# Optimization experiments

Measured on AMD Instinct MI355X. Metric: run time of the kernel, lower is better.

## Reference

```python
import jax, jax.numpy as jnp
import numpy as np

B, FEW, NN = 4096, 5, 64
D = 128            # embed_dim
NSYM = 100000
DM = 2 * D         # d_model = 256
DI = 2 * DM        # support-encoder inner = 512
H = 2 * DM         # LSTMCell hidden = 512
STEPS = 4          # process_steps


def setup_inputs() -> dict:
    key = jax.random.key(0)
    cnt = [0]
    def nk():
        cnt[0] += 1
        return jax.random.fold_in(key, cnt[0])
    def nrm(shape, scale=0.05):
        return jax.random.normal(nk(), shape, dtype=jnp.float32) * scale
    def ridx(shape):
        return jax.random.randint(nk(), shape, 0, NSYM, dtype=jnp.int32)
    inp = {}
    inp['q_l1'] = ridx((B, NN, 2)); inp['q_l2'] = ridx((B, NN, 2))
    inp['q_r1'] = ridx((B, NN, 2)); inp['q_r2'] = ridx((B, NN, 2))
    inp['s_l1'] = ridx((FEW, NN, 2)); inp['s_l2'] = ridx((FEW, NN, 2))
    inp['s_r1'] = ridx((FEW, NN, 2)); inp['s_r2'] = ridx((FEW, NN, 2))
    inp['q_deg_l'] = jax.random.randint(nk(), (B,), 1, NN, dtype=jnp.int32)
    inp['q_deg_r'] = jax.random.randint(nk(), (B,), 1, NN, dtype=jnp.int32)
    inp['s_deg_l'] = jax.random.randint(nk(), (FEW,), 1, NN, dtype=jnp.int32)
    inp['s_deg_r'] = jax.random.randint(nk(), (FEW,), 1, NN, dtype=jnp.int32)
    inp['emb'] = nrm((NSYM + 1, D)).at[NSYM].set(0.0)  # padding_idx row = 0
    inp['gcn_w'] = nrm((D, 2 * D))
    inp['gcn_wb'] = nrm((D,))
    inp['gcn_b'] = jnp.zeros((D,), jnp.float32)
    inp['hop_gate'] = jnp.ones((2,), jnp.float32)
    inp['attn_w'] = nrm((1, D))
    inp['attn_b'] = jnp.zeros((1,), jnp.float32)
    inp['p1_w'] = nrm((DI, DM)); inp['p1_b'] = jnp.zeros((DI,), jnp.float32)
    inp['p2_w'] = nrm((DM, DI)); inp['p2_b'] = jnp.zeros((DM,), jnp.float32)
    inp['ln_g'] = jnp.ones((DM,), jnp.float32); inp['ln_b'] = jnp.zeros((DM,), jnp.float32)
    inp['w_ih'] = nrm((4 * H, DM)); inp['w_hh'] = nrm((4 * H, H))
    inp['b_ih'] = jnp.zeros((4 * H,), jnp.float32); inp['b_hh'] = jnp.zeros((4 * H,), jnp.float32)
    return inp


def _neighbor_encoder(conn, emb, gcn_w, gcn_wb, gcn_b, attn_w, attn_b):
    # conn: [N, NN, 2] (relation id, entity id)
    e = emb[conn]                                     # [N, NN, 2, D]
    concat = e.reshape(conn.shape[0], conn.shape[1], 2 * D)  # cat(rel, ent)
    proj = concat @ gcn_w.T + gcn_wb + gcn_b          # [N, NN, D]
    scores = (proj @ attn_w.T + attn_b)[..., 0]       # [N, NN]
    w = jax.nn.softmax(scores, axis=1)[..., None]
    return jnp.tanh(jnp.sum(proj * w, axis=1))        # [N, D]


def _support_encoder(x, p1_w, p1_b, p2_w, p2_b, ln_g, ln_b):
    out = jax.nn.relu(x @ p1_w.T + p1_b) @ p2_w.T + p2_b
    z = out + x
    mu = jnp.mean(z, axis=-1, keepdims=True)
    var = jnp.var(z, axis=-1, keepdims=True)
    return (z - mu) / jnp.sqrt(var + 1e-6) * ln_g + ln_b


def _query_encoder(support_g, q, w_ih, w_hh, b_ih, b_hh):
    # matching-networks 'process' LSTM attention, STEPS fixed iterations
    h_r = jnp.zeros((q.shape[0], H), q.dtype)
    c = jnp.zeros_like(h_r)
    h = q
    for _ in range(STEPS):
        gates = q @ w_ih.T + b_ih + h_r @ w_hh.T + b_hh
        i, f, g, o = jnp.split(gates, 4, axis=-1)
        c = jax.nn.sigmoid(f) * c + jax.nn.sigmoid(i) * jnp.tanh(g)
        h_cell = jax.nn.sigmoid(o) * jnp.tanh(c)
        h = q + h_cell[:, :DM]
        attn = jax.nn.softmax(h @ support_g.T, axis=1)
        r = attn @ support_g
        h_r = jnp.concatenate([h, r], axis=1)
    return h


def reference(q_l1, q_l2, q_r1, q_r2, s_l1, s_l2, s_r1, s_r2,
              q_deg_l, q_deg_r, s_deg_l, s_deg_r,
              emb, gcn_w, gcn_wb, gcn_b, hop_gate, attn_w, attn_b,
              p1_w, p1_b, p2_w, p2_b, ln_g, ln_b, w_ih, w_hh, b_ih, b_hh):
    ne = lambda conn: _neighbor_encoder(conn, emb, gcn_w, gcn_wb, gcn_b, attn_w, attn_b)
    gw = jax.nn.softmax(hop_gate)
    q_left = gw[0] * ne(q_l1) + gw[1] * ne(q_l2)
    q_right = gw[0] * ne(q_r1) + gw[1] * ne(q_r2)
    s_left = gw[0] * ne(s_l1) + gw[1] * ne(s_l2)
    s_right = gw[0] * ne(s_r1) + gw[1] * ne(s_r2)
    query_neighbor = jnp.concatenate([q_left, q_right], axis=-1)    # [B, DM]
    support_neighbor = jnp.concatenate([s_left, s_right], axis=-1)  # [FEW, DM]
    support_g = _support_encoder(support_neighbor, p1_w, p1_b, p2_w, p2_b, ln_g, ln_b)
    query_g = _query_encoder(support_g, query_neighbor, w_ih, w_hh, b_ih, b_hh)
    support_m = jnp.mean(support_g, axis=0, keepdims=True)          # [1, DM]
    return (query_g @ support_m.T)[:, 0]                            # [B]
```

## Files before the change

kernel.cpp:

```cpp
#include <hip/hip_runtime.h>

typedef unsigned short bf16u;
typedef unsigned char u8;
typedef unsigned int u32;
typedef float f32x4 __attribute__((ext_vector_type(4)));
typedef short bf16x8 __attribute__((ext_vector_type(8)));

__device__ inline float sigmoidf_(float x) { return 1.f / (1.f + __expf(-x)); }
__device__ inline float tanhf_(float x) {
  float e = __expf(2.f * x);
  return 1.f - 2.f / (e + 1.f);
}
__device__ inline float b2f(bf16u u) { return __uint_as_float(((u32)u) << 16); }
__device__ inline bf16u f2b(float f) {
  u32 i = __float_as_uint(f);
  u32 r = (i + 0x7fffu + ((i >> 16) & 1u)) >> 16;
  return (bf16u)r;
}
__device__ inline u8 enc8(float v) {
  float q = fmaf(v, 512.f, 128.5f);
  q = fminf(fmaxf(q, 0.f), 255.f);
  return (u8)(int)q;
}
__device__ inline float ub0(u32 u) { return (float)(u & 0xffu); }
__device__ inline float ub1(u32 u) { return (float)((u >> 8) & 0xffu); }
__device__ inline float ub2(u32 u) { return (float)((u >> 16) & 0xffu); }
__device__ inline float ub3(u32 u) { return (float)(u >> 24); }

#define GLOAD16(gsrc, ldst)                                                   \
  __builtin_amdgcn_global_load_lds(                                           \
      (const __attribute__((address_space(1))) void*)(gsrc),                  \
      (__attribute__((address_space(3))) void*)(ldst), 16, 0, 0)

__global__ __launch_bounds__(256) void k_prep(
    const float* __restrict__ gcn_w, const float* __restrict__ attn_w,
    const float* __restrict__ w_ih, const float* __restrict__ w_hh,
    const float* __restrict__ b_ih, const float* __restrict__ b_hh,
    bf16u* __restrict__ Vp, float* __restrict__ uvec,
    bf16u* __restrict__ WWa, bf16u* __restrict__ WWb, float* __restrict__ bsum,
    bf16u* __restrict__ XX)
{
  const int b = blockIdx.x, t = threadIdx.x;
  if (t < 59) XX[(size_t)b * 576 + 517 + t] = 0;
  if (b < 2048) {
    float wi = w_ih[b * 256 + t];
    float wh = w_hh[b * 512 + t];
    WWa[(size_t)b * 576 + t] = f2b(wi);
    WWb[(size_t)b * 576 + t] = f2b(wi + wh);
    WWb[(size_t)b * 576 + 256 + t] = f2b(wh);
    if (t < 59) WWb[(size_t)b * 576 + 517 + t] = 0;
    if (t == 0) bsum[b] = b_ih[b] + b_hh[b];
  } else if (b < 2304) {
    const int o = b - 2048;
    if (t < 128) Vp[o * 128 + t] = f2b(gcn_w[(o & 127) * 256 + ((o >> 7) << 7) + t]);
  } else if (b == 2304) {
    const int col = ((t >> 7) << 7) + (t & 127);
    float acc = 0.f;
    for (int d = 0; d < 128; ++d) acc += gcn_w[d * 256 + col] * attn_w[d];
    uvec[t] = acc;
  }
}

__global__ __launch_bounds__(256) void k_pre_gemm(
    const float* __restrict__ emb, const bf16u* __restrict__ Vp,
    const float* __restrict__ uvec,
    u8* __restrict__ pr, u8* __restrict__ pe,
    float* __restrict__ srel, float* __restrict__ sent)
{
  const int t = threadIdx.x;
  const int row0 = blockIdx.x << 6;
  __shared__ short As[64][136];
  __shared__ union PB {
    short B[128][136];
    u8 ob[64][272];
  } pb;
  __shared__ float us[256];
  us[t] = uvec[t];
  {
    const uint4* src = (const uint4*)Vp;
    #pragma unroll
    for (int s = 0; s < 8; ++s) {
      int f = s * 256 + t;
      *(uint4*)&pb.B[f >> 4][(f & 15) * 8] = src[f];
    }
  }
  #pragma unroll
  for (int s = 0; s < 8; ++s) {
    int f = s * 256 + t;
    int row = f >> 5, q = f & 31;
    int gr = row0 + row; if (gr > 100000) gr = 100000;
    float4 v = *(const float4*)&emb[(size_t)gr * 128 + (q << 2)];
    ushort4 pk;
    pk.x = f2b(v.x); pk.y = f2b(v.y); pk.z = f2b(v.z); pk.w = f2b(v.w);
    *(ushort4*)&As[row][q << 2] = pk;
  }
  __syncthreads();
  {
    const int row = t >> 2, l = t & 3;
    int gr = row0 + row; if (gr > 100000) gr = 100000;
    const short* ar = &As[row][l * 32];
    const float* u0 = &us[l * 32];
    const float* u1 = &us[128 + l * 32];
    float p0 = 0.f, p1 = 0.f;
    #pragma unroll
    for (int i = 0; i < 32; ++i) {
      float e = __uint_as_float(((u32)(unsigned short)ar[i]) << 16);
      p0 += e * u0[i];
      p1 += e * u1[i];
    }
    p0 += __shfl_xor(p0, 1, 64); p0 += __shfl_xor(p0, 2, 64);
    p1 += __shfl_xor(p1, 1, 64); p1 += __shfl_xor(p1, 2, 64);
    if (l == 0) { srel[gr] = p0; sent[gr] = p1; }
  }
  const int wave = t >> 6, lane = t & 63;
  const int quad = lane >> 4, l16 = lane & 15;
  const int wm = (wave >> 1) << 5, wn = (wave & 1) << 6;
  f32x4 acc0[2][4], acc1[2][4];
  #pragma unroll
  for (int i = 0; i < 2; ++i)
    #pragma unroll
    for (int j = 0; j < 4; ++j) {
      acc0[i][j] = (f32x4){0.f, 0.f, 0.f, 0.f};
      acc1[i][j] = (f32x4){0.f, 0.f, 0.f, 0.f};
    }
  #pragma unroll
  for (int kc = 0; kc < 4; ++kc) {
    bf16x8 af[2], bfr[4];
    #pragma unroll
    for (int i = 0; i < 2; ++i)
      af[i] = *(const bf16x8*)&As[wm + i * 16 + l16][kc * 32 + quad * 8];
    #pragma unroll
    for (int j = 0; j < 4; ++j)
      bfr[j] = *(const bf16x8*)&pb.B[wn + j * 16 + l16][kc * 32 + quad * 8];
    #pragma unroll
    for (int i = 0; i < 2; ++i)
      #pragma unroll
      for (int j = 0; j < 4; ++j)
        acc0[i][j] = __builtin_amdgcn_mfma_f32_16x16x32_bf16(af[i], bfr[j], acc0[i][j], 0, 0, 0);
  }
  __syncthreads();
  {
    const uint4* src = (const uint4*)(Vp + 128 * 128);
    #pragma unroll
    for (int s = 0; s < 8; ++s) {
      int f = s * 256 + t;
      *(uint4*)&pb.B[f >> 4][(f & 15) * 8] = src[f];
    }
  }
  __syncthreads();
  #pragma unroll
  for (int kc = 0; kc < 4; ++kc) {
    bf16x8 af[2], bfr[4];
    #pragma unroll
    for (int i = 0; i < 2; ++i)
      af[i] = *(const bf16x8*)&As[wm + i * 16 + l16][kc * 32 + quad * 8];
    #pragma unroll
    for (int j = 0; j < 4; ++j)
      bfr[j] = *(const bf16x8*)&pb.B[wn + j * 16 + l16][kc * 32 + quad * 8];
    #pragma unroll
    for (int i = 0; i < 2; ++i)
      #pragma unroll
      for (int j = 0; j < 4; ++j)
        acc1[i][j] = __builtin_amdgcn_mfma_f32_16x16x32_bf16(af[i], bfr[j], acc1[i][j], 0, 0, 0);
  }
  __syncthreads();
  #pragma unroll
  for (int j = 0; j < 4; ++j) {
    const int col = wn + j * 16 + l16;
    #pragma unroll
    for (int i = 0; i < 2; ++i) {
      #pragma unroll
      for (int r = 0; r < 4; ++r) {
        int row = wm + i * 16 + quad * 4 + r;
        pb.ob[row][col] = enc8(acc0[i][j][r]);
        pb.ob[row][128 + col] = enc8(acc1[i][j][r]);
      }
    }
  }
  __syncthreads();
  #pragma unroll
  for (int s = 0; s < 4; ++s) {
    int c = s * 256 + t;
    int row = c >> 4, part = c & 15;
    int gr = row0 + row;
    if (gr <= 100000) {
      uint4 v = *(const uint4*)&pb.ob[row][part * 16];
      if (part < 8) *(uint4*)&pr[(size_t)gr * 128 + part * 16] = v;
      else          *(uint4*)&pe[(size_t)gr * 128 + (part - 8) * 16] = v;
    }
  }
}

__global__ __launch_bounds__(256) void k_neighbor(
    const int* __restrict__ q_l1, const int* __restrict__ q_l2,
    const int* __restrict__ q_r1, const int* __restrict__ q_r2,
    const int* __restrict__ s_l1, const int* __restrict__ s_l2,
    const int* __restrict__ s_r1, const int* __restrict__ s_r2,
    const u8* __restrict__ pr, const u8* __restrict__ pe,
    const float* __restrict__ srel, const float* __restrict__ sent,
    const float* __restrict__ gcn_wb, const float* __restrict__ gcn_b,
    const float* __restrict__ hop_gate,
    float* __restrict__ qn, float* __restrict__ sn, bf16u* __restrict__ XX)
{
  const int b = blockIdx.x, t = threadIdx.x;
  const int *cA, *cB; float* outp; bf16u* xxp; int n, coloff;
  if (b < 4096)      { cA = q_l1; cB = q_l2; n = b;        outp = qn; xxp = XX; coloff = 0; }
  else if (b < 8192) { cA = q_r1; cB = q_r2; n = b - 4096; outp = qn; xxp = XX; coloff = 128; }
  else if (b < 8197) { cA = s_l1; cB = s_l2; n = b - 8192; outp = sn; xxp = 0;  coloff = 0; }
  else               { cA = s_r1; cB = s_r2; n = b - 8197; outp = sn; xxp = 0;  coloff = 128; }

  __shared__ float wS[2][64];
  __shared__ float red[256][17];

  const int hop = t >> 7, g = (t >> 3) & 15, p = t & 7;
  const int* connG = hop ? cB : cA;

  int2 pairs[4];
  #pragma unroll
  for (int kk = 0; kk < 4; ++kk)
    pairs[kk] = *(const int2*)&connG[(n * 64 + g + (kk << 4)) * 2];

  float vR = 0.f, vE = 0.f;
  if (t < 128) {
    const int sh = t >> 6, nn = t & 63;
    const int* connS = sh ? cB : cA;
    int2 sp = *(const int2*)&connS[(n * 64 + nn) * 2];
    vR = srel[sp.x];
    vE = sent[sp.y];
  }

  uint4 ra[4], rb[4];
  #pragma unroll
  for (int kk = 0; kk < 4; ++kk) {
    ra[kk] = *(const uint4*)&pr[(size_t)pairs[kk].x * 128 + p * 16];
    rb[kk] = *(const uint4*)&pe[(size_t)pairs[kk].y * 128 + p * 16];
  }

  if (t < 128) {
    const int sh = t >> 6, nn = t & 63;
    float sc = vR + vE;
    float m = sc;
    #pragma unroll
    for (int off = 32; off; off >>= 1) m = fmaxf(m, __shfl_xor(m, off, 64));
    float e = __expf(sc - m);
    float s = e;
    #pragma unroll
    for (int off = 32; off; off >>= 1) s += __shfl_xor(s, off, 64);
    wS[sh][nn] = e / s;
  }
  __syncthreads();

  float a[16];
  #pragma unroll
  for (int c = 0; c < 16; ++c) a[c] = 0.f;
  #pragma unroll
  for (int kk = 0; kk < 4; ++kk) {
    const float wk = wS[hop][g + (kk << 4)];
    const uint4 A = ra[kk], Bv = rb[kk];
    a[0]  += wk * (ub0(A.x) + ub0(Bv.x));
    a[1]  += wk * (ub1(A.x) + ub1(Bv.x));
    a[2]  += wk * (ub2(A.x) + ub2(Bv.x));
    a[3]  += wk * (ub3(A.x) + ub3(Bv.x));
    a[4]  += wk * (ub0(A.y) + ub0(Bv.y));
    a[5]  += wk * (ub1(A.y) + ub1(Bv.y));
    a[6]  += wk * (ub2(A.y) + ub2(Bv.y));
    a[7]  += wk * (ub3(A.y) + ub3(Bv.y));
    a[8]  += wk * (ub0(A.z) + ub0(Bv.z));
    a[9]  += wk * (ub1(A.z) + ub1(Bv.z));
    a[10] += wk * (ub2(A.z) + ub2(Bv.z));
    a[11] += wk * (ub3(A.z) + ub3(Bv.z));
    a[12] += wk * (ub0(A.w) + ub0(Bv.w));
    a[13] += wk * (ub1(A.w) + ub1(Bv.w));
    a[14] += wk * (ub2(A.w) + ub2(Bv.w));
    a[15] += wk * (ub3(A.w) + ub3(Bv.w));
  }
  #pragma unroll
  for (int c = 0; c < 16; ++c) red[t][c] = a[c];
  __syncthreads();

  if (t < 128) {
    const int d = t, pp = d >> 4, cc = d & 15;
    float sA = 0.f, sB = 0.f;
    #pragma unroll
    for (int gg = 0; gg < 16; ++gg) {
      sA += red[gg * 8 + pp][cc];
      sB += red[128 + gg * 8 + pp][cc];
    }
    float accA = sA * (1.f / 512.f) - 0.5f;
    float accB = sB * (1.f / 512.f) - 0.5f;
    float bias = gcn_wb[d] + gcn_b[d];
    float g0 = hop_gate[0], g1 = hop_gate[1];
    float mx = fmaxf(g0, g1);
    float e0 = __expf(g0 - mx), e1 = __expf(g1 - mx);
    float inv = 1.f / (e0 + e1);
    float v = e0 * inv * tanhf_(bias + accA) + e1 * inv * tanhf_(bias + accB);
    outp[n * 256 + coloff + d] = v;
    if (xxp) xxp[(size_t)n * 576 + coloff + d] = f2b(v);
  }
}

__global__ __launch_bounds__(256) void k_sup1(
    const float* __restrict__ sn, const float* __restrict__ p1_w,
    const float* __restrict__ p1_b, float* __restrict__ h1)
{
  const int r = blockIdx.x >> 3, j0 = (blockIdx.x & 7) << 6;
  const int t = threadIdx.x;
  __shared__ float xs[256];
  xs[t] = sn[r * 256 + t];
  __syncthreads();
  const int j = j0 + (t >> 2), q = t & 3;
  const float* wr = p1_w + (size_t)j * 256 + q * 64;
  float acc = 0.f;
  #pragma unroll
  for (int k = 0; k < 64; ++k) acc += xs[q * 64 + k] * wr[k];
  acc += __shfl_xor(acc, 1, 64);
  acc += __shfl_xor(acc, 2, 64);
  if (q == 0) h1[r * 512 + j] = fmaxf(acc + p1_b[j], 0.f);
}

__global__ __launch_bounds__(256) void k_sup2(
    const float* __restrict__ sn, const float* __restrict__ h1,
    const float* __restrict__ p2_w, const float* __restrict__ p2_b,
    const float* __restrict__ ln_g, const float* __restrict__ ln_b,
    float* __restrict__ sg)
{
  const int r = blockIdx.x, t = threadIdx.x;
  const int lane = t & 63, wave = t >> 6;
  __shared__ float hs[512];
  __shared__ float zs[256];
  __shared__ float r1[4], r2[4];
  hs[t] = h1[r * 512 + t];
  hs[t + 256] = h1[r * 512 + 256 + t];
  __syncthreads();
  const int q = t & 3;
  #pragma unroll
  for (int jc = 0; jc < 4; ++jc) {
    int j = jc * 64 + (t >> 2);
    const float* wr = p2_w + (size_t)j * 512 + q * 128;
    float acc = 0.f;
    #pragma unroll
    for (int k = 0; k < 128; ++k) acc += hs[q * 128 + k] * wr[k];
    acc += __shfl_xor(acc, 1, 64);
    acc += __shfl_xor(acc, 2, 64);
    if (q == 0) zs[j] = acc + p2_b[j] + sn[r * 256 + j];
  }
  __syncthreads();
  float v = zs[t];
  float s1 = v, s2 = v * v;
  #pragma unroll
  for (int off = 32; off; off >>= 1) { s1 += __shfl_xor(s1, off, 64); s2 += __shfl_xor(s2, off, 64); }
  if (lane == 0) { r1[wave] = s1; r2[wave] = s2; }
  __syncthreads();
  float S1 = r1[0] + r1[1] + r1[2] + r1[3];
  float S2 = r2[0] + r2[1] + r2[2] + r2[3];
  float mu = S1 * (1.f / 256.f);
  float var = S2 * (1.f / 256.f) - mu * mu;
  sg[r * 256 + t] = (v - mu) * rsqrtf(var + 1e-6f) * ln_g[t] + ln_b[t];
}

__global__ __launch_bounds__(256) void k_sg2(
    const float* __restrict__ sg, const float* __restrict__ w_hh,
    bf16u* __restrict__ WWb, float* __restrict__ sm)
{
  __shared__ float s[5][256];
  const int t = threadIdx.x;
  for (int i = t; i < 1280; i += 256) s[i >> 8][i & 255] = sg[i];
  __syncthreads();
  if (blockIdx.x == 0)
    sm[t] = (s[0][t] + s[1][t] + s[2][t] + s[3][t] + s[4][t]) * 0.2f;
  const int j = (blockIdx.x << 6) + (t >> 2), q = t & 3;
  const float4* wr = (const float4*)(w_hh + (size_t)j * 512 + 256 + q * 64);
  float a[5] = {0.f, 0.f, 0.f, 0.f, 0.f};
  #pragma unroll
  for (int kk = 0; kk < 16; ++kk) {
    float4 w = wr[kk];
    int k = q * 64 + kk * 4;
    #pragma unroll
    for (int r = 0; r < 5; ++r)
      a[r] += s[r][k] * w.x + s[r][k+1] * w.y + s[r][k+2] * w.z + s[r][k+3] * w.w;
  }
  #pragma unroll
  for (int r = 0; r < 5; ++r) {
    a[r] += __shfl_xor(a[r], 1, 64);
    a[r] += __shfl_xor(a[r], 2, 64);
  }
  if (q == 0) {
    #pragma unroll
    for (int r = 0; r < 5; ++r)
      WWb[(size_t)j * 576 + 512 + r] = f2b(a[r]);
  }
}

__global__ __launch_bounds__(256) void k_gates_mfma(
    const bf16u* __restrict__ XX, const bf16u* __restrict__ WW,
    const float* __restrict__ bsum, bf16u* __restrict__ gates, int kchunks)
{
  const int t = threadIdx.x;
  const int wave = t >> 6, lane = t & 63;
  const int quad = lane >> 4, l16 = lane & 15;
  const int wm = (wave >> 1) << 6, wn = (wave & 1) << 6;
  const int lin = (blockIdx.x & 7) * 56 + (blockIdx.x >> 3);
  const int row0 = (lin / 14) << 7;
  const int col0 = (lin % 14) << 7;
  __shared__ short As[2][128][32];
  __shared__ short Bs[2][128][32];
  f32x4 acc[4][4];
  #pragma unroll
  for (int i = 0; i < 4; ++i)
    #pragma unroll
    for (int j = 0; j < 4; ++j) acc[i][j] = (f32x4){0.f, 0.f, 0.f, 0.f};

  int offX[2], offW[2];
  #pragma unroll
  for (int e = 0; e < 2; ++e) {
    int s = wave * 128 + e * 64 + lane;
    int row = s >> 2, qs = s & 3;
    int sw = qs ^ ((row >> 1) & 3);
    offX[e] = (row0 + row) * 576 + sw * 8;
    offW[e] = (col0 + row) * 576 + sw * 8;
  }
  char* aBase = (char*)&As[0][0][0] + wave * 2048;
  char* bBase = (char*)&Bs[0][0][0] + wave * 2048;

  #define STAGE(buf, kc)                                                      \
    {                                                                         \
      const int kof_ = (kc) * 32;                                             \
      _Pragma("unroll")                                                       \
      for (int e = 0; e < 2; ++e) {                                           \
        GLOAD16(XX + offX[e] + kof_, aBase + (buf) * 8192 + e * 1024);        \
        GLOAD16(WW + offW[e] + kof_, bBase + (buf) * 8192 + e * 1024);        \
      }                                                                       \
    }

  STAGE(0, 0);
  __syncthreads();

  const int swq = (quad ^ ((l16 >> 1) & 3)) << 3;
  for (int kc = 0; kc < kchunks; ++kc) {
    const int cur = kc & 1;
    if (kc + 1 < kchunks) STAGE(cur ^ 1, kc + 1);
    bf16x8 af[4], bfr[4];
    #pragma unroll
    for (int i = 0; i < 4; ++i)
      af[i] = *(const bf16x8*)&As[cur][wm + i * 16 + l16][swq];
    #pragma unroll
    for (int j = 0; j < 4; ++j)
      bfr[j] = *(const bf16x8*)&Bs[cur][wn + j * 16 + l16][swq];
    #pragma unroll
    for (int i = 0; i < 4; ++i)
      #pragma unroll
      for (int j = 0; j < 4; ++j)
        acc[i][j] = __builtin_amdgcn_mfma_f32_16x16x32_bf16(af[i], bfr[j], acc[i][j], 0, 0, 0);
    __syncthreads();
  }
  #undef STAGE

  #pragma unroll
  for (int j = 0; j < 4; ++j) {
    const int col = col0 + wn + j * 16 + l16;
    const float bs = bsum[col];
    #pragma unroll
    for (int i = 0; i < 4; ++i) {
      #pragma unroll
      for (int r = 0; r < 4; ++r) {
        int row = row0 + wm + i * 16 + quad * 4 + r;
        gates[(size_t)row * 2048 + col] = f2b(acc[i][j][r] + bs);
      }
    }
  }
}

__global__ __launch_bounds__(256) void k_cell(
    const bf16u* __restrict__ gates, const float* __restrict__ qn,
    float* __restrict__ c, bf16u* __restrict__ XX,
    const float* __restrict__ sg, const float* __restrict__ sm,
    float* __restrict__ out, int step)
{
  __shared__ float red[4][6];
  const int b = blockIdx.x, t = threadIdx.x;
  const int lane = t & 63, wave = t >> 6;
  const bf16u* g = gates + (size_t)b * 2048;
  float i0 = b2f(g[t]),       f0 = b2f(g[512 + t]), gg0 = b2f(g[1024 + t]), o0 = b2f(g[1536 + t]);
  float i1 = b2f(g[256 + t]), f1 = b2f(g[768 + t]), gg1 = b2f(g[1280 + t]);
  float co0 = step ? c[b * 512 + t] : 0.f;
  float co1 = step ? c[b * 512 + 256 + t] : 0.f;
  float c0 = sigmoidf_(f0) * co0 + sigmoidf_(i0) * tanhf_(gg0);
  float c1 = sigmoidf_(f1) * co1 + sigmoidf_(i1) * tanhf_(gg1);
  if (step < 3) {
    c[b * 512 + t] = c0;
    c[b * 512 + 256 + t] = c1;
  }
  float hcv = sigmoidf_(o0) * tanhf_(c0);
  float h = qn[b * 256 + t] + hcv;
  if (step < 3) {
    XX[(size_t)b * 576 + 256 + t] = f2b(hcv);
    float dots[5];
    #pragma unroll
    for (int s = 0; s < 5; ++s) dots[s] = h * sg[s * 256 + t];
    #pragma unroll
    for (int off = 32; off; off >>= 1) {
      #pragma unroll
      for (int s = 0; s < 5; ++s) dots[s] += __shfl_xor(dots[s], off, 64);
    }
    if (lane == 0) {
      #pragma unroll
      for (int s = 0; s < 5; ++s) red[wave][s] = dots[s];
    }
    __syncthreads();
    #pragma unroll
    for (int s = 0; s < 5; ++s)
      dots[s] = red[0][s] + red[1][s] + red[2][s] + red[3][s];
    float m = dots[0];
    #pragma unroll
    for (int s = 1; s < 5; ++s) m = fmaxf(m, dots[s]);
    float sum = 0.f;
    #pragma unroll
    for (int s = 0; s < 5; ++s) sum += __expf(dots[s] - m);
    if (t < 5) {
      float dv = (t == 1) ? dots[1] : (t == 2) ? dots[2] : (t == 3) ? dots[3]
               : (t == 4) ? dots[4] : dots[0];
      XX[(size_t)b * 576 + 512 + t] = f2b(__expf(dv - m) / sum);
    }
  } else {
    float v = h * sm[t];
    #pragma unroll
    for (int off = 32; off; off >>= 1) v += __shfl_xor(v, off, 64);
    if (lane == 0) red[wave][0] = v;
    __syncthreads();
    if (t == 0) out[b] = red[0][0] + red[1][0] + red[2][0] + red[3][0];
  }
}

extern "C" void kernel_launch(void* const* d_in, const int* in_sizes, int n_in,
                              void* d_out, int out_size, void* d_ws, size_t ws_size,
                              hipStream_t stream)
{
  (void)in_sizes; (void)n_in; (void)out_size; (void)ws_size;
  const int *q_l1 = (const int*)d_in[0], *q_l2 = (const int*)d_in[1];
  const int *q_r1 = (const int*)d_in[2], *q_r2 = (const int*)d_in[3];
  const int *s_l1 = (const int*)d_in[4], *s_l2 = (const int*)d_in[5];
  const int *s_r1 = (const int*)d_in[6], *s_r2 = (const int*)d_in[7];
  const float* emb      = (const float*)d_in[12];
  const float* gcn_w    = (const float*)d_in[13];
  const float* gcn_wb   = (const float*)d_in[14];
  const float* gcn_b    = (const float*)d_in[15];
  const float* hop_gate = (const float*)d_in[16];
  const float* attn_w   = (const float*)d_in[17];
  const float* p1_w = (const float*)d_in[19];
  const float* p1_b = (const float*)d_in[20];
  const float* p2_w = (const float*)d_in[21];
  const float* p2_b = (const float*)d_in[22];
  const float* ln_g = (const float*)d_in[23];
  const float* ln_b = (const float*)d_in[24];
  const float* w_ih = (const float*)d_in[25];
  const float* w_hh = (const float*)d_in[26];
  const float* b_ih = (const float*)d_in[27];
  const float* b_hh = (const float*)d_in[28];

  char* base = (char*)d_ws;
  size_t off = 0;
  auto alloc = [&](size_t bytes) -> char* {
    char* r = base + off;
    off = (off + bytes + 255) & ~(size_t)255;
    return r;
  };
  u8* pr       = (u8*)alloc(100001ull * 128);
  u8* pe       = (u8*)alloc(100001ull * 128);
  float* srel  = (float*)alloc(100001ull * 4);
  float* sent  = (float*)alloc(100001ull * 4);
  float* uvec  = (float*)alloc(256 * 4);
  bf16u* Vp    = (bf16u*)alloc(256 * 128 * 2);
  float* qn    = (float*)alloc(4096ull * 256 * 4);
  float* sn    = (float*)alloc(5 * 256 * 4);
  float* sg    = (float*)alloc(5 * 256 * 4);
  float* sm    = (float*)alloc(256 * 4);
  float* h1b   = (float*)alloc(5 * 512 * 4);
  bf16u* XX    = (bf16u*)alloc(4096ull * 576 * 2);
  bf16u* WWa   = (bf16u*)alloc(2048ull * 576 * 2);
  bf16u* WWb   = (bf16u*)alloc(2048ull * 576 * 2);
  float* bsum  = (float*)alloc(2048 * 4);
  bf16u* gates = (bf16u*)alloc(4096ull * 2048 * 2);
  float* cbuf  = (float*)alloc(4096ull * 512 * 4);

  k_prep<<<4096, 256, 0, stream>>>(gcn_w, attn_w, w_ih, w_hh, b_ih, b_hh,
                                   Vp, uvec, WWa, WWb, bsum, XX);
  k_pre_gemm<<<1563, 256, 0, stream>>>(emb, Vp, uvec, pr, pe, srel, sent);
  k_neighbor<<<8202, 256, 0, stream>>>(q_l1, q_l2, q_r1, q_r2, s_l1, s_l2, s_r1, s_r2,
                                       pr, pe, srel, sent, gcn_wb, gcn_b, hop_gate,
                                       qn, sn, XX);
  k_sup1<<<40, 256, 0, stream>>>(sn, p1_w, p1_b, h1b);
  k_sup2<<<5, 256, 0, stream>>>(sn, h1b, p2_w, p2_b, ln_g, ln_b, sg);
  k_sg2<<<32, 256, 0, stream>>>(sg, w_hh, WWb, sm);

  for (int step = 0; step < 4; ++step) {
    if (step == 0)
      k_gates_mfma<<<448, 256, 0, stream>>>(XX, WWa, bsum, gates, 8);
    else
      k_gates_mfma<<<448, 256, 0, stream>>>(XX, WWb, bsum, gates, 17);
    k_cell<<<4096, 256, 0, stream>>>(gates, qn, cbuf, XX, sg, sm, (float*)d_out, step);
  }
}
```

Measured before the change: 334.8 us.

## Merge prep and pre-GEMM kernels and deepen the gates GEMM K tile

Folds the weight-prep kernel into the embedding pre-GEMM kernel as one launch. Each pre-GEMM block now recomputes the attention projection vector and converts gcn_w to bf16 in shared memory itself, instead of reading precomputed buffers. The LSTM gates MFMA GEMM now stages 64-wide K chunks (double-buffered, with a new XOR swizzle) instead of 32, halving the loop iterations and barriers. This costs twice the LDS and some redundant per-block weight work.

```diff
diff --git a/kernel.cpp b/kernel.cpp
--- a/kernel.cpp
+++ b/kernel.cpp
@@ -32,17 +32,23 @@
       (const __attribute__((address_space(1))) void*)(gsrc),                  \
       (__attribute__((address_space(3))) void*)(ldst), 16, 0, 0)
 
-__global__ __launch_bounds__(256) void k_prep(
-    const float* __restrict__ gcn_w, const float* __restrict__ attn_w,
+__global__ __launch_bounds__(256) void k_front(
+    const float* __restrict__ emb, const float* __restrict__ gcn_w,
+    const float* __restrict__ attn_w,
     const float* __restrict__ w_ih, const float* __restrict__ w_hh,
     const float* __restrict__ b_ih, const float* __restrict__ b_hh,
-    bf16u* __restrict__ Vp, float* __restrict__ uvec,
+    u8* __restrict__ pr, u8* __restrict__ pe,
+    float* __restrict__ srel, float* __restrict__ sent,
     bf16u* __restrict__ WWa, bf16u* __restrict__ WWb, float* __restrict__ bsum,
     bf16u* __restrict__ XX)
 {
-  const int b = blockIdx.x, t = threadIdx.x;
-  if (t < 59) XX[(size_t)b * 576 + 517 + t] = 0;
-  if (b < 2048) {
+  const int blk = blockIdx.x, t = threadIdx.x;
+  if (blk >= 1563) {
+    const int b = blk - 1563;
+    if (t < 59) {
+      XX[(size_t)b * 576 + 517 + t] = 0;
+      XX[(size_t)(b + 2048) * 576 + 517 + t] = 0;
+    }
     float wi = w_ih[b * 256 + t];
     float wh = w_hh[b * 512 + t];
     WWa[(size_t)b * 576 + t] = f2b(wi);
@@ -50,38 +56,33 @@
     WWb[(size_t)b * 576 + 256 + t] = f2b(wh);
     if (t < 59) WWb[(size_t)b * 576 + 517 + t] = 0;
     if (t == 0) bsum[b] = b_ih[b] + b_hh[b];
-  } else if (b < 2304) {
-    const int o = b - 2048;
-    if (t < 128) Vp[o * 128 + t] = f2b(gcn_w[(o & 127) * 256 + ((o >> 7) << 7) + t]);
-  } else if (b == 2304) {
-    const int col = ((t >> 7) << 7) + (t & 127);
-    float acc = 0.f;
-    for (int d = 0; d < 128; ++d) acc += gcn_w[d * 256 + col] * attn_w[d];
-    uvec[t] = acc;
-  }
-}
-
-__global__ __launch_bounds__(256) void k_pre_gemm(
-    const float* __restrict__ emb, const bf16u* __restrict__ Vp,
-    const float* __restrict__ uvec,
-    u8* __restrict__ pr, u8* __restrict__ pe,
-    float* __restrict__ srel, float* __restrict__ sent)
-{
-  const int t = threadIdx.x;
-  const int row0 = blockIdx.x << 6;
+    return;
+  }
+  const int row0 = blk << 6;
   __shared__ short As[64][136];
   __shared__ union PB {
     short B[128][136];
     u8 ob[64][272];
   } pb;
   __shared__ float us[256];
-  us[t] = uvec[t];
   {
-    const uint4* src = (const uint4*)Vp;
+    float acc = 0.f;
+    #pragma unroll 8
+    for (int d = 0; d < 128; ++d) acc = fmaf(gcn_w[d * 256 + t], attn_w[d], acc);
+    us[t] = acc;
+  }
+  {
     #pragma unroll
     for (int s = 0; s < 8; ++s) {
       int f = s * 256 + t;
-      *(uint4*)&pb.B[f >> 4][(f & 15) * 8] = src[f];
+      int row = f >> 4, e0 = (f & 15) * 8;
+      float4 v0 = *(const float4*)&gcn_w[row * 256 + e0];
+      float4 v1 = *(const float4*)&gcn_w[row * 256 + e0 + 4];
+      ushort4 p0, p1;
+      p0.x = f2b(v0.x); p0.y = f2b(v0.y); p0.z = f2b(v0.z); p0.w = f2b(v0.w);
+      p1.x = f2b(v1.x); p1.y = f2b(v1.y); p1.z = f2b(v1.z); p1.w = f2b(v1.w);
+      *(ushort4*)&pb.B[row][e0] = p0;
+      *(ushort4*)&pb.B[row][e0 + 4] = p1;
     }
   }
   #pragma unroll
@@ -140,11 +141,17 @@
   }
   __syncthreads();
   {
-    const uint4* src = (const uint4*)(Vp + 128 * 128);
     #pragma unroll
     for (int s = 0; s < 8; ++s) {
       int f = s * 256 + t;
-      *(uint4*)&pb.B[f >> 4][(f & 15) * 8] = src[f];
+      int row = f >> 4, e0 = (f & 15) * 8;
+      float4 v0 = *(const float4*)&gcn_w[row * 256 + 128 + e0];
+      float4 v1 = *(const float4*)&gcn_w[row * 256 + 128 + e0 + 4];
+      ushort4 p0, p1;
+      p0.x = f2b(v0.x); p0.y = f2b(v0.y); p0.z = f2b(v0.z); p0.w = f2b(v0.w);
+      p1.x = f2b(v1.x); p1.y = f2b(v1.y); p1.z = f2b(v1.z); p1.w = f2b(v1.w);
+      *(ushort4*)&pb.B[row][e0] = p0;
+      *(ushort4*)&pb.B[row][e0 + 4] = p1;
     }
   }
   __syncthreads();
@@ -402,55 +409,58 @@
   const int lin = (blockIdx.x & 7) * 56 + (blockIdx.x >> 3);
   const int row0 = (lin / 14) << 7;
   const int col0 = (lin % 14) << 7;
-  __shared__ short As[2][128][32];
-  __shared__ short Bs[2][128][32];
+  __shared__ short As[2][128][64];
+  __shared__ short Bs[2][128][64];
   f32x4 acc[4][4];
   #pragma unroll
   for (int i = 0; i < 4; ++i)
     #pragma unroll
     for (int j = 0; j < 4; ++j) acc[i][j] = (f32x4){0.f, 0.f, 0.f, 0.f};
 
-  int offX[2], offW[2];
-  #pragma unroll
-  for (int e = 0; e < 2; ++e) {
-    int s = wave * 128 + e * 64 + lane;
-    int row = s >> 2, qs = s & 3;
-    int sw = qs ^ ((row >> 1) & 3);
+  int offX[4], offW[4];
+  #pragma unroll
+  for (int e = 0; e < 4; ++e) {
+    int row = wave * 32 + e * 8 + (lane >> 3);
+    int sw = (lane & 7) ^ (lane >> 3);
     offX[e] = (row0 + row) * 576 + sw * 8;
     offW[e] = (col0 + row) * 576 + sw * 8;
   }
-  char* aBase = (char*)&As[0][0][0] + wave * 2048;
-  char* bBase = (char*)&Bs[0][0][0] + wave * 2048;
+  char* aBase = (char*)&As[0][0][0] + wave * 4096;
+  char* bBase = (char*)&Bs[0][0][0] + wave * 4096;
 
   #define STAGE(buf, kc)                                                      \
     {                                                                         \
-      const int kof_ = (kc) * 32;                                             \
+      const int kof_ = (kc) * 64;                                             \
       _Pragma("unroll")                                                       \
-      for (int e = 0; e < 2; ++e) {                                           \
-        GLOAD16(XX + offX[e] + kof_, aBase + (buf) * 8192 + e * 1024);        \
-        GLOAD16(WW + offW[e] + kof_, bBase + (buf) * 8192 + e * 1024);        \
+      for (int e = 0; e < 4; ++e) {                                           \
+        GLOAD16(XX + offX[e] + kof_, aBase + (buf) * 16384 + e * 1024);       \
+        GLOAD16(WW + offW[e] + kof_, bBase + (buf) * 16384 + e * 1024);       \
       }                                                                       \
     }
 
   STAGE(0, 0);
   __syncthreads();
 
-  const int swq = (quad ^ ((l16 >> 1) & 3)) << 3;
   for (int kc = 0; kc < kchunks; ++kc) {
     const int cur = kc & 1;
     if (kc + 1 < kchunks) STAGE(cur ^ 1, kc + 1);
-    bf16x8 af[4], bfr[4];
-    #pragma unroll
-    for (int i = 0; i < 4; ++i)
-      af[i] = *(const bf16x8*)&As[cur][wm + i * 16 + l16][swq];
-    #pragma unroll
-    for (int j = 0; j < 4; ++j)
-      bfr[j] = *(const bf16x8*)&Bs[cur][wn + j * 16 + l16][swq];
-    #pragma unroll
-    for (int i = 0; i < 4; ++i)
+    #pragma unroll
+    for (int kc2 = 0; kc2 < 2; ++kc2) {
+      bf16x8 af[4], bfr[4];
+      #pragma unroll
+      for (int i = 0; i < 4; ++i)
+        af[i] = *(const bf16x8*)&As[cur][wm + i * 16 + l16]
+                                       [(((kc2 << 2) + quad) ^ (l16 & 7)) << 3];
       #pragma unroll
       for (int j = 0; j < 4; ++j)
-        acc[i][j] = __builtin_amdgcn_mfma_f32_16x16x32_bf16(af[i], bfr[j], acc[i][j], 0, 0, 0);
+        bfr[j] = *(const bf16x8*)&Bs[cur][wn + j * 16 + l16]
+                                        [(((kc2 << 2) + quad) ^ (l16 & 7)) << 3];
+      #pragma unroll
+      for (int i = 0; i < 4; ++i)
+        #pragma unroll
+        for (int j = 0; j < 4; ++j)
+          acc[i][j] = __builtin_amdgcn_mfma_f32_16x16x32_bf16(af[i], bfr[j], acc[i][j], 0, 0, 0);
+    }
     __syncthreads();
   }
   #undef STAGE
@@ -568,8 +578,6 @@
   u8* pe       = (u8*)alloc(100001ull * 128);
   float* srel  = (float*)alloc(100001ull * 4);
   float* sent  = (float*)alloc(100001ull * 4);
-  float* uvec  = (float*)alloc(256 * 4);
-  bf16u* Vp    = (bf16u*)alloc(256 * 128 * 2);
   float* qn    = (float*)alloc(4096ull * 256 * 4);
   float* sn    = (float*)alloc(5 * 256 * 4);
   float* sg    = (float*)alloc(5 * 256 * 4);
@@ -582,9 +590,8 @@
   bf16u* gates = (bf16u*)alloc(4096ull * 2048 * 2);
   float* cbuf  = (float*)alloc(4096ull * 512 * 4);
 
-  k_prep<<<4096, 256, 0, stream>>>(gcn_w, attn_w, w_ih, w_hh, b_ih, b_hh,
-                                   Vp, uvec, WWa, WWb, bsum, XX);
-  k_pre_gemm<<<1563, 256, 0, stream>>>(emb, Vp, uvec, pr, pe, srel, sent);
+  k_front<<<3611, 256, 0, stream>>>(emb, gcn_w, attn_w, w_ih, w_hh, b_ih, b_hh,
+                                    pr, pe, srel, sent, WWa, WWb, bsum, XX);
   k_neighbor<<<8202, 256, 0, stream>>>(q_l1, q_l2, q_r1, q_r2, s_l1, s_l2, s_r1, s_r2,
                                        pr, pe, srel, sent, gcn_wb, gcn_b, hop_gate,
                                        qn, sn, XX);
@@ -594,9 +601,9 @@
 
   for (int step = 0; step < 4; ++step) {
     if (step == 0)
-      k_gates_mfma<<<448, 256, 0, stream>>>(XX, WWa, bsum, gates, 8);
+      k_gates_mfma<<<448, 256, 0, stream>>>(XX, WWa, bsum, gates, 4);
     else
-      k_gates_mfma<<<448, 256, 0, stream>>>(XX, WWb, bsum, gates, 17);
+      k_gates_mfma<<<448, 256, 0, stream>>>(XX, WWb, bsum, gates, 9);
     k_cell<<<4096, 256, 0, stream>>>(gates, qn, cbuf, XX, sg, sm, (float*)d_out, step);
   }
 }
```

Measured after the change: 335.7 us. Within noise of the previous version (+0.3%).
